# Kernel tuning notes

Measured on AMD Instinct MI355X. Metric: run time of the kernel, lower is better.

## Reference

```python
import jax, jax.numpy as jnp
import numpy as np

ANCHORS = np.array([[116., 90.], [156., 198.], [373., 326.],
                    [30., 61.], [62., 45.], [59., 119.],
                    [10., 13.], [16., 30.], [33., 23.]], dtype=np.float32)
IMG_WH = (416.0, 416.0)  # image_size[::-1]
IGNORE_THRESH = 0.5
MAX_BOXES = 64  # static upper bound on true boxes per image per layer


def bce_logits(t, x):
    # tf.nn.sigmoid_cross_entropy_with_logits(labels=t, logits=x)
    return jnp.maximum(x, 0.0) - x * t + jnp.log1p(jnp.exp(-jnp.abs(x)))


def box_iou(b1, b2):
    # b1: [B,H,W,3,4] xywh, b2: [B,M,4] xywh -> iou [B,H,W,3,M]
    b1 = b1[..., None, :]
    b2 = b2[:, None, None, None, :, :]
    b1_min = b1[..., :2] - b1[..., 2:4] * 0.5
    b1_max = b1[..., :2] + b1[..., 2:4] * 0.5
    b2_min = b2[..., :2] - b2[..., 2:4] * 0.5
    b2_max = b2[..., :2] + b2[..., 2:4] * 0.5
    inter_wh = jnp.maximum(jnp.minimum(b1_max, b2_max) - jnp.maximum(b1_min, b2_min), 0.0)
    inter = inter_wh[..., 0] * inter_wh[..., 1]
    a1 = b1[..., 2] * b1[..., 3]
    a2 = b2[..., 2] * b2[..., 3]
    return inter / (a1 + a2 - inter)


def layer_loss(yt, pred, anchors):
    # yt: [B,H,W,3,5+C], pred: [B,H,W,3*(5+C)]
    B, H, W = yt.shape[:3]
    C = pred.shape[-1] // 3 - 5
    p = pred.reshape(B, H, W, 3, 5 + C)
    gy, gx = jnp.meshgrid(jnp.arange(H), jnp.arange(W), indexing='ij')
    grid = jnp.stack([gx, gy], -1).astype(pred.dtype)[:, :, None, :]  # [H,W,1,2]
    fwh = jnp.array([W, H], pred.dtype)
    anc = anchors.reshape(1, 1, 1, 3, 2)
    # pred_process (channel layout: 0=conf, 1:3=xy, 3:5=wh, 5:=class)
    xy = (jax.nn.sigmoid(p[..., 1:3]) + grid) / fwh
    wh = jnp.exp(p[..., 3:5]) * anc / fwh
    conf = jax.nn.sigmoid(p[..., 0:1])
    cls = jax.nn.sigmoid(p[..., 5:])
    pred_box = jnp.concatenate([xy, wh], -1)

    obj = yt[..., 0:1]
    true_cls = yt[..., 5:]
    true_xy = yt[..., 1:3] * fwh - grid
    true_wh = jnp.log(yt[..., 3:5] / anc * jnp.array(IMG_WH, yt.dtype))
    true_wh = jnp.where(obj > 0, true_wh, jnp.zeros_like(true_wh))
    scale = 2.0 - yt[..., 3:4] * yt[..., 4:5]

    # vectorized replacement for the per-image while_loop + boolean_mask:
    # gather the MAX_BOXES highest-objectness cells per image as candidate true boxes
    flat_obj = obj[..., 0].reshape(B, -1)
    flat_box = yt[..., 1:5].reshape(B, -1, 4)
    vals, idx = jax.lax.top_k(flat_obj, MAX_BOXES)
    tboxes = jnp.take_along_axis(flat_box, idx[..., None], axis=1)  # [B,M,4]
    iou = box_iou(pred_box, tboxes)                                 # [B,H,W,3,M]
    iou = jnp.where((vals > 0.5)[:, None, None, None, :], iou, -jnp.inf)
    best_iou = jnp.max(iou, axis=-1)  # -inf when no true boxes (matches tf reduce_max over empty)
    ignore = (best_iou < IGNORE_THRESH).astype(yt.dtype)[..., None]

    xy_l = obj * scale * bce_logits(true_xy, xy)
    wh_l = obj * scale * 0.5 * jnp.square(true_wh - wh)
    conf_l = obj * bce_logits(obj, conf) + (1.0 - obj) * bce_logits(obj, conf) * ignore
    cls_l = obj * bce_logits(true_cls, cls)
    red = lambda t: jnp.sum(t, axis=(1, 2, 3, 4))
    return red(xy_l) + red(wh_l) + red(conf_l) + red(cls_l)


def yolo_loss(y_true, p0, p1, p2):
    B, _, A, D = y_true.shape
    yts = [y_true[:, 0:169].reshape(B, 13, 13, A, D),
           y_true[:, 169:845].reshape(B, 26, 26, A, D),
           y_true[:, 845:3549].reshape(B, 52, 52, A, D)]
    anc = jnp.asarray(ANCHORS)
    total = jnp.zeros((B,), y_true.dtype)
    for i, pred in enumerate([p0, p1, p2]):
        total = total + layer_loss(yts[i], pred, anc[3 * i:3 * i + 3])
    return total


def setup_inputs() -> dict:
    key = jax.random.key(0)
    B, N, C = 32, 3549, 80
    k1, k2, k3, k4, k5, k6, k7 = jax.random.split(key, 7)
    obj = (jax.random.uniform(k1, (B, N, 3, 1)) < 0.002).astype(jnp.float32)
    xy = jax.random.uniform(k2, (B, N, 3, 2), minval=0.05, maxval=0.95)
    wh = jax.random.uniform(k3, (B, N, 3, 2), minval=0.05, maxval=0.4)
    cls = (jax.random.uniform(k4, (B, N, 3, C)) < (1.0 / C)).astype(jnp.float32)
    y_true = jnp.concatenate([obj, xy, wh, cls], axis=-1)
    pred_13 = 0.5 * jax.random.normal(k5, (B, 13, 13, 255), dtype=jnp.float32)
    pred_26 = 0.5 * jax.random.normal(k6, (B, 26, 26, 255), dtype=jnp.float32)
    pred_52 = 0.5 * jax.random.normal(k7, (B, 52, 52, 255), dtype=jnp.float32)
    return {"y_true": y_true, "pred_13": pred_13, "pred_26": pred_26, "pred_52": pred_52}


def reference(y_true, pred_13, pred_26, pred_52):
    return yolo_loss(y_true, pred_13, pred_26, pred_52)
```

## Files before the change

### kernel.cpp

```cpp
#include <hip/hip_runtime.h>

#define NPAIR 96
#define MAXB 64
#define CAP 256

__constant__ float c_anc[9][2] = {
    {116.f, 90.f}, {156.f, 198.f}, {373.f, 326.f},
    { 30.f, 61.f}, { 62.f, 45.f}, { 59.f, 119.f},
    { 10.f, 13.f}, { 16.f, 30.f}, { 33.f, 23.f}};

typedef float floatx4 __attribute__((ext_vector_type(4), aligned(4)));

__device__ __forceinline__ float sigm(float x) { return 1.f / (1.f + expf(-x)); }

__device__ __forceinline__ float bce_f(float t, float x) {
    return fmaxf(x, 0.f) - x * t + logf(1.f + expf(-fabsf(x)));
}

__device__ __forceinline__ void map_block(int j, int& l, int& blk, int& S) {
    if (j < 2)       { l = 0; blk = j;      S = 13; }
    else if (j < 10) { l = 1; blk = j - 2;  S = 26; }
    else             { l = 2; blk = j - 10; S = 52; }
}

template <int ITERS>
__device__ __forceinline__ void scan_obj(const float* __restrict__ ybase,
                                         int nCells, int tid,
                                         unsigned long long* swords) {
    float ov[ITERS];
#pragma unroll
    for (int k = 0; k < ITERS; ++k) {
        int c = tid + (k << 8);
        ov[k] = (c < nCells) ? ybase[(long long)c * 85] : 0.f;
    }
    int lane = tid & 63, wv = tid >> 6;
#pragma unroll
    for (int k = 0; k < ITERS; ++k) {
        unsigned long long m = __ballot(ov[k] > 0.5f);
        if (lane == 0) swords[k * 4 + wv] = m;
    }
}

__global__ __launch_bounds__(256) void prep_k(
    const float* __restrict__ yt,
    const float* __restrict__ p13, const float* __restrict__ p26,
    const float* __restrict__ p52,
    float4* __restrict__ oboxes, int* __restrict__ counts,
    unsigned long long* __restrict__ bmp_all,
    float* __restrict__ posloss, float* __restrict__ out)
{
    int pair = blockIdx.x;
    int tid = threadIdx.x;
    int b = pair / 3;
    int l = pair - b * 3;
    int S      = (l == 0) ? 13  : (l == 1) ? 26  : 52;
    int n0     = (l == 0) ? 0   : (l == 1) ? 169 : 845;
    int nwords = (l == 0) ? 8   : (l == 1) ? 32  : 128;
    int nCells = S * S * 3;
    float Sf = (float)S;
    const float* ybase = yt + (long long)(b * 3549 + n0) * 255;
    const float* pred  = (l == 0) ? p13 : (l == 1) ? p26 : p52;
    const float* pbase = pred + (long long)b * S * S * 255;

    if (pair == 0 && tid < 32) out[tid] = 0.f;

    __shared__ unsigned long long swords[128];
    __shared__ int sidx[CAP];
    __shared__ int sbase[2];
    __shared__ int stot_s;
    __shared__ float pls[4];

    if (l == 0)      scan_obj<2 >(ybase, nCells, tid, swords);
    else if (l == 1) scan_obj<8 >(ybase, nCells, tid, swords);
    else             scan_obj<32>(ybase, nCells, tid, swords);
    __syncthreads();

    int lane = tid & 63, wv = tid >> 6;
    unsigned long long w = 0ULL;
    int pc = 0;
    if (tid < 128) {
        w = (tid < nwords) ? swords[tid] : 0ULL;
        pc = __popcll(w);
    }
    int x = pc;
#pragma unroll
    for (int d = 1; d < 64; d <<= 1) {
        int y = __shfl_up(x, d, 64);
        if (lane >= d) x += y;
    }
    if (tid < 128 && lane == 63) sbase[wv] = x;
    if (tid < nwords) bmp_all[(long long)pair * 128 + tid] = w;
    __syncthreads();
    if (tid == 0) stot_s = sbase[0] + sbase[1];
    if (tid < 128) {
        int base = x - pc + (wv ? sbase[0] : 0);
        unsigned long long ww = w;
        while (ww) {
            int bit = __ffsll((long long)ww) - 1;
            if (base < CAP) sidx[base] = tid * 64 + bit;
            ++base;
            ww &= ww - 1;
        }
    }
    __syncthreads();

    int stot = stot_s;
    int TC = stot < CAP ? stot : CAP;
    int MB = TC < MAXB ? TC : MAXB;
    if (tid == 0) counts[pair] = MB;
    if (tid < MB) {
        int idx = sidx[tid];
        const float* yc = ybase + (long long)idx * 85;
        oboxes[pair * MAXB + tid] = make_float4(yc[1], yc[2], yc[3], yc[4]);
    }

    float wsum = 0.f;
    for (int i = wv; i < TC; i += 4) {
        int idx = sidx[i];
        const float* yc = ybase + (long long)idx * 85;
        const float* pc_ = pbase + (long long)idx * 85;
        float part = bce_f(yc[5 + lane], sigm(pc_[5 + lane]));
        if (lane < 16)
            part += bce_f(yc[69 + lane], sigm(pc_[69 + lane]));
        if (lane == 0) {
            int p_ = idx / 3, a = idx - p_ * 3;
            int gh = p_ / S, gw = p_ - gh * S;
            float aw = c_anc[l * 3 + a][0], ah = c_anc[l * 3 + a][1];
            float v0 = pc_[0], v1 = pc_[1], v2 = pc_[2], v3 = pc_[3], v4 = pc_[4];
            float t1 = yc[1], t2 = yc[2], t3 = yc[3], t4 = yc[4];
            part += bce_f(1.f, sigm(v0));
            float sc = 2.f - t3 * t4;
            float px = (sigm(v1) + (float)gw) / Sf;
            float py = (sigm(v2) + (float)gh) / Sf;
            part += sc * (bce_f(t1 * Sf - (float)gw, px) +
                          bce_f(t2 * Sf - (float)gh, py));
            float pw = expf(v3) * aw / Sf, ph = expf(v4) * ah / Sf;
            float twx = logf(t3 / aw * 416.f), twy = logf(t4 / ah * 416.f);
            part += sc * 0.5f * ((twx - pw) * (twx - pw) + (twy - ph) * (twy - ph));
        }
#pragma unroll
        for (int off = 32; off > 0; off >>= 1)
            part += __shfl_down(part, off, 64);
        if (lane == 0) wsum += part;
    }
    if (lane == 0) pls[wv] = wsum;
    __syncthreads();
    if (tid == 0) posloss[pair] = pls[0] + pls[1] + pls[2] + pls[3];
}

__global__ __launch_bounds__(256) void neg_k(
    const float* __restrict__ p13, const float* __restrict__ p26,
    const float* __restrict__ p52,
    const float4* __restrict__ oboxes, const int* __restrict__ counts,
    const unsigned long long* __restrict__ bmp_all,
    const float* __restrict__ posloss, float* __restrict__ out)
{
    int bid = blockIdx.x;
    int tid = threadIdx.x;
    int b = bid / 42;
    int j = bid - b * 42;
    int l, blk, S;
    map_block(j, l, blk, S);
    int nCells = S * S * 3;
    int pair = b * 3 + l;
    float Sf = (float)S;
    const float* pred  = (l == 0) ? p13 : (l == 1) ? p26 : p52;
    const float* pbase = pred + (long long)b * S * S * 255;

    __shared__ float sxmin[MAXB], sxmax[MAXB], symin[MAXB], symax[MAXB], sba[MAXB];
    int count = counts[pair];
    if (tid < count) {
        float4 g = oboxes[pair * MAXB + tid];
        sxmin[tid] = g.x - g.z * 0.5f;
        sxmax[tid] = g.x + g.z * 0.5f;
        symin[tid] = g.y - g.w * 0.5f;
        symax[tid] = g.y + g.w * 0.5f;
        sba[tid]   = g.z * g.w;
    }
    __syncthreads();

    float loss = 0.f;
    int c = blk * 256 + tid;
    if (c < nCells) {
        unsigned long long word = bmp_all[(long long)pair * 128 + (c >> 6)];
        if (!((word >> (c & 63)) & 1ULL)) {
            const float* pc = pbase + (long long)c * 85;
            floatx4 v03 = *(const floatx4*)pc;
            float v0 = v03.x;
            if (count == 0) {
                loss = bce_f(0.f, sigm(v0));
            } else {
                float v4 = pc[4];
                int p_ = c / 3, a = c - p_ * 3;
                int gh = p_ / S, gw = p_ - gh * S;
                float aw = c_anc[l * 3 + a][0], ah = c_anc[l * 3 + a][1];
                float px = (sigm(v03.y) + (float)gw) / Sf;
                float py = (sigm(v03.z) + (float)gh) / Sf;
                float pw = expf(v03.w) * aw / Sf, ph = expf(v4) * ah / Sf;
                float pxmin = px - pw * 0.5f, pxmax = px + pw * 0.5f;
                float pymin = py - ph * 0.5f, pymax = py + ph * 0.5f;
                float parea = pw * ph;
                bool hit = false;
#pragma unroll 4
                for (int i = 0; i < count; ++i) {
                    float iw = fminf(pxmax, sxmax[i]) - fmaxf(pxmin, sxmin[i]);
                    float ih = fminf(pymax, symax[i]) - fmaxf(pymin, symin[i]);
                    float inter = fmaxf(iw, 0.f) * fmaxf(ih, 0.f);
                    hit = hit || (3.f * inter >= parea + sba[i]);
                }
                if (!hit) loss = bce_f(0.f, sigm(v0));
            }
        }
    }
    if (tid == 0 && blk == 0) loss += posloss[pair];

#pragma unroll
    for (int off = 32; off > 0; off >>= 1)
        loss += __shfl_down(loss, off, 64);
    __shared__ float wsum[4];
    if ((tid & 63) == 0) wsum[tid >> 6] = loss;
    __syncthreads();
    if (tid == 0)
        atomicAdd(out + b, wsum[0] + wsum[1] + wsum[2] + wsum[3]);
}

extern "C" void kernel_launch(void* const* d_in, const int* in_sizes, int n_in,
                              void* d_out, int out_size, void* d_ws, size_t ws_size,
                              hipStream_t stream) {
    (void)in_sizes; (void)n_in; (void)out_size; (void)ws_size;
    const float* yt  = (const float*)d_in[0];
    const float* p13 = (const float*)d_in[1];
    const float* p26 = (const float*)d_in[2];
    const float* p52 = (const float*)d_in[3];
    float* out = (float*)d_out;

    unsigned long long* bmp = (unsigned long long*)d_ws;
    float4* oboxes = (float4*)((char*)d_ws + NPAIR * 128 * 8);
    int* counts    = (int*)((char*)d_ws + NPAIR * 128 * 8 + NPAIR * MAXB * 16);
    float* posloss = (float*)((char*)d_ws + NPAIR * 128 * 8 + NPAIR * MAXB * 16
                              + NPAIR * sizeof(int));

    prep_k<<<NPAIR, 256, 0, stream>>>(yt, p13, p26, p52, oboxes, counts, bmp,
                                      posloss, out);
    neg_k<<<32 * 42, 256, 0, stream>>>(p13, p26, p52, oboxes, counts, bmp,
                                       posloss, out);
}
```

Baseline: 259.8 us.

## Fuse prep and negative-loss kernels, recomputing objectness scan per block

Merges the two-kernel pipeline into one kernel launched over 1344 blocks. Each block redoes the per-(image, layer) objectness scan and box gather in shared memory instead of reading them from a workspace written by a 96-block prep kernel. The positive-cell loss is computed only by block 0 of each pair. This removes the serial, low-occupancy prep stage and the workspace round trip, but repeats the strided y_true scan in every block of a layer (up to 32 blocks for the 52x52 layer). It also switches to fast __expf, __logf and rcp intrinsics and adds a tiny init kernel to zero the output.

```diff
diff --git a/kernel.cpp b/kernel.cpp
--- a/kernel.cpp
+++ b/kernel.cpp
@@ -1,6 +1,5 @@
 #include <hip/hip_runtime.h>
 
-#define NPAIR 96
 #define MAXB 64
 #define CAP 256
 
@@ -11,89 +10,88 @@
 
 typedef float floatx4 __attribute__((ext_vector_type(4), aligned(4)));
 
-__device__ __forceinline__ float sigm(float x) { return 1.f / (1.f + expf(-x)); }
-
+__device__ __forceinline__ float sigm(float x) {
+    return __builtin_amdgcn_rcpf(1.f + __expf(-x));
+}
 __device__ __forceinline__ float bce_f(float t, float x) {
-    return fmaxf(x, 0.f) - x * t + logf(1.f + expf(-fabsf(x)));
+    return fmaxf(x, 0.f) - x * t + __logf(1.f + __expf(-fabsf(x)));
 }
 
-__device__ __forceinline__ void map_block(int j, int& l, int& blk, int& S) {
-    if (j < 2)       { l = 0; blk = j;      S = 13; }
-    else if (j < 10) { l = 1; blk = j - 2;  S = 26; }
-    else             { l = 2; blk = j - 10; S = 52; }
+__device__ __forceinline__ void map_block(int j, int& l, int& blk, int& S,
+                                          int& n0, int& nwords) {
+    if (j < 2)       { l = 0; blk = j;      S = 13; n0 = 0;   nwords = 8;   }
+    else if (j < 10) { l = 1; blk = j - 2;  S = 26; n0 = 169; nwords = 32;  }
+    else             { l = 2; blk = j - 10; S = 52; n0 = 845; nwords = 128; }
 }
 
 template <int ITERS>
 __device__ __forceinline__ void scan_obj(const float* __restrict__ ybase,
-                                         int nCells, int tid,
+                                         int nCells, int lane, int wv,
                                          unsigned long long* swords) {
     float ov[ITERS];
 #pragma unroll
     for (int k = 0; k < ITERS; ++k) {
-        int c = tid + (k << 8);
+        int c = (((k << 2) + wv) << 6) + lane;
         ov[k] = (c < nCells) ? ybase[(long long)c * 85] : 0.f;
     }
-    int lane = tid & 63, wv = tid >> 6;
 #pragma unroll
     for (int k = 0; k < ITERS; ++k) {
         unsigned long long m = __ballot(ov[k] > 0.5f);
-        if (lane == 0) swords[k * 4 + wv] = m;
+        if (lane == 0) swords[(k << 2) + wv] = m;
     }
 }
 
-__global__ __launch_bounds__(256) void prep_k(
+__global__ void init_k(float* __restrict__ out) { out[threadIdx.x] = 0.f; }
+
+__global__ __launch_bounds__(256) void loss_k(
     const float* __restrict__ yt,
     const float* __restrict__ p13, const float* __restrict__ p26,
-    const float* __restrict__ p52,
-    float4* __restrict__ oboxes, int* __restrict__ counts,
-    unsigned long long* __restrict__ bmp_all,
-    float* __restrict__ posloss, float* __restrict__ out)
+    const float* __restrict__ p52, float* __restrict__ out)
 {
-    int pair = blockIdx.x;
-    int tid = threadIdx.x;
-    int b = pair / 3;
-    int l = pair - b * 3;
-    int S      = (l == 0) ? 13  : (l == 1) ? 26  : 52;
-    int n0     = (l == 0) ? 0   : (l == 1) ? 169 : 845;
-    int nwords = (l == 0) ? 8   : (l == 1) ? 32  : 128;
+    int bid = blockIdx.x, tid = threadIdx.x;
+    int b = bid / 42, j = bid - b * 42;
+    int l, blk, S, n0, nwords;
+    map_block(j, l, blk, S, n0, nwords);
     int nCells = S * S * 3;
     float Sf = (float)S;
+    float invS = __builtin_amdgcn_rcpf(Sf);
     const float* ybase = yt + (long long)(b * 3549 + n0) * 255;
     const float* pred  = (l == 0) ? p13 : (l == 1) ? p26 : p52;
     const float* pbase = pred + (long long)b * S * S * 255;
+    int lane = tid & 63, wv = tid >> 6;
 
-    if (pair == 0 && tid < 32) out[tid] = 0.f;
+    int c = blk * 256 + tid;
+    bool act = c < nCells;
+    int cc = act ? c : 0;
+    const float* pcp = pbase + (long long)cc * 85;
+    floatx4 v03 = *(const floatx4*)pcp;
+    float v4 = pcp[4];
 
     __shared__ unsigned long long swords[128];
     __shared__ int sidx[CAP];
-    __shared__ int sbase[2];
+    __shared__ int sbase2[2];
     __shared__ int stot_s;
-    __shared__ float pls[4];
+    __shared__ float sxmin[MAXB], sxmax[MAXB], symin[MAXB], symax[MAXB], sba[MAXB];
 
-    if (l == 0)      scan_obj<2 >(ybase, nCells, tid, swords);
-    else if (l == 1) scan_obj<8 >(ybase, nCells, tid, swords);
-    else             scan_obj<32>(ybase, nCells, tid, swords);
+    if (l == 0)      scan_obj<2 >(ybase, nCells, lane, wv, swords);
+    else if (l == 1) scan_obj<8 >(ybase, nCells, lane, wv, swords);
+    else             scan_obj<32>(ybase, nCells, lane, wv, swords);
     __syncthreads();
 
-    int lane = tid & 63, wv = tid >> 6;
     unsigned long long w = 0ULL;
     int pc = 0;
-    if (tid < 128) {
-        w = (tid < nwords) ? swords[tid] : 0ULL;
-        pc = __popcll(w);
-    }
+    if (tid < 128) { w = (tid < nwords) ? swords[tid] : 0ULL; pc = __popcll(w); }
     int x = pc;
 #pragma unroll
     for (int d = 1; d < 64; d <<= 1) {
         int y = __shfl_up(x, d, 64);
         if (lane >= d) x += y;
     }
-    if (tid < 128 && lane == 63) sbase[wv] = x;
-    if (tid < nwords) bmp_all[(long long)pair * 128 + tid] = w;
+    if (tid < 128 && lane == 63) sbase2[wv] = x;
     __syncthreads();
-    if (tid == 0) stot_s = sbase[0] + sbase[1];
+    if (tid == 0) stot_s = sbase2[0] + sbase2[1];
     if (tid < 128) {
-        int base = x - pc + (wv ? sbase[0] : 0);
+        int base = x - pc + (wv ? sbase2[0] : 0);
         unsigned long long ww = w;
         while (ww) {
             int bit = __ffsll((long long)ww) - 1;
@@ -107,141 +105,95 @@
     int stot = stot_s;
     int TC = stot < CAP ? stot : CAP;
     int MB = TC < MAXB ? TC : MAXB;
-    if (tid == 0) counts[pair] = MB;
     if (tid < MB) {
         int idx = sidx[tid];
+        if (idx >= nCells) idx = nCells - 1;
         const float* yc = ybase + (long long)idx * 85;
-        oboxes[pair * MAXB + tid] = make_float4(yc[1], yc[2], yc[3], yc[4]);
-    }
-
-    float wsum = 0.f;
-    for (int i = wv; i < TC; i += 4) {
-        int idx = sidx[i];
-        const float* yc = ybase + (long long)idx * 85;
-        const float* pc_ = pbase + (long long)idx * 85;
-        float part = bce_f(yc[5 + lane], sigm(pc_[5 + lane]));
-        if (lane < 16)
-            part += bce_f(yc[69 + lane], sigm(pc_[69 + lane]));
-        if (lane == 0) {
-            int p_ = idx / 3, a = idx - p_ * 3;
-            int gh = p_ / S, gw = p_ - gh * S;
-            float aw = c_anc[l * 3 + a][0], ah = c_anc[l * 3 + a][1];
-            float v0 = pc_[0], v1 = pc_[1], v2 = pc_[2], v3 = pc_[3], v4 = pc_[4];
-            float t1 = yc[1], t2 = yc[2], t3 = yc[3], t4 = yc[4];
-            part += bce_f(1.f, sigm(v0));
-            float sc = 2.f - t3 * t4;
-            float px = (sigm(v1) + (float)gw) / Sf;
-            float py = (sigm(v2) + (float)gh) / Sf;
-            part += sc * (bce_f(t1 * Sf - (float)gw, px) +
-                          bce_f(t2 * Sf - (float)gh, py));
-            float pw = expf(v3) * aw / Sf, ph = expf(v4) * ah / Sf;
-            float twx = logf(t3 / aw * 416.f), twy = logf(t4 / ah * 416.f);
-            part += sc * 0.5f * ((twx - pw) * (twx - pw) + (twy - ph) * (twy - ph));
-        }
-#pragma unroll
-        for (int off = 32; off > 0; off >>= 1)
-            part += __shfl_down(part, off, 64);
-        if (lane == 0) wsum += part;
-    }
-    if (lane == 0) pls[wv] = wsum;
-    __syncthreads();
-    if (tid == 0) posloss[pair] = pls[0] + pls[1] + pls[2] + pls[3];
-}
-
-__global__ __launch_bounds__(256) void neg_k(
-    const float* __restrict__ p13, const float* __restrict__ p26,
-    const float* __restrict__ p52,
-    const float4* __restrict__ oboxes, const int* __restrict__ counts,
-    const unsigned long long* __restrict__ bmp_all,
-    const float* __restrict__ posloss, float* __restrict__ out)
-{
-    int bid = blockIdx.x;
-    int tid = threadIdx.x;
-    int b = bid / 42;
-    int j = bid - b * 42;
-    int l, blk, S;
-    map_block(j, l, blk, S);
-    int nCells = S * S * 3;
-    int pair = b * 3 + l;
-    float Sf = (float)S;
-    const float* pred  = (l == 0) ? p13 : (l == 1) ? p26 : p52;
-    const float* pbase = pred + (long long)b * S * S * 255;
-
-    __shared__ float sxmin[MAXB], sxmax[MAXB], symin[MAXB], symax[MAXB], sba[MAXB];
-    int count = counts[pair];
-    if (tid < count) {
-        float4 g = oboxes[pair * MAXB + tid];
-        sxmin[tid] = g.x - g.z * 0.5f;
-        sxmax[tid] = g.x + g.z * 0.5f;
-        symin[tid] = g.y - g.w * 0.5f;
-        symax[tid] = g.y + g.w * 0.5f;
-        sba[tid]   = g.z * g.w;
+        float gx = yc[1], gy = yc[2], gww = yc[3], ghh = yc[4];
+        sxmin[tid] = gx - gww * 0.5f; sxmax[tid] = gx + gww * 0.5f;
+        symin[tid] = gy - ghh * 0.5f; symax[tid] = gy + ghh * 0.5f;
+        sba[tid]   = gww * ghh;
     }
     __syncthreads();
 
-    float loss = 0.f;
-    int c = blk * 256 + tid;
-    if (c < nCells) {
-        unsigned long long word = bmp_all[(long long)pair * 128 + (c >> 6)];
-        if (!((word >> (c & 63)) & 1ULL)) {
-            const float* pc = pbase + (long long)c * 85;
-            floatx4 v03 = *(const floatx4*)pc;
-            float v0 = v03.x;
-            if (count == 0) {
-                loss = bce_f(0.f, sigm(v0));
-            } else {
-                float v4 = pc[4];
-                int p_ = c / 3, a = c - p_ * 3;
-                int gh = p_ / S, gw = p_ - gh * S;
-                float aw = c_anc[l * 3 + a][0], ah = c_anc[l * 3 + a][1];
-                float px = (sigm(v03.y) + (float)gw) / Sf;
-                float py = (sigm(v03.z) + (float)gh) / Sf;
-                float pw = expf(v03.w) * aw / Sf, ph = expf(v4) * ah / Sf;
-                float pxmin = px - pw * 0.5f, pxmax = px + pw * 0.5f;
-                float pymin = py - ph * 0.5f, pymax = py + ph * 0.5f;
-                float parea = pw * ph;
-                bool hit = false;
-#pragma unroll 4
-                for (int i = 0; i < count; ++i) {
-                    float iw = fminf(pxmax, sxmax[i]) - fmaxf(pxmin, sxmin[i]);
-                    float ih = fminf(pymax, symax[i]) - fmaxf(pymin, symin[i]);
-                    float inter = fmaxf(iw, 0.f) * fmaxf(ih, 0.f);
-                    hit = hit || (3.f * inter >= parea + sba[i]);
-                }
-                if (!hit) loss = bce_f(0.f, sigm(v0));
+    int p_ = cc / 3, a = cc - p_ * 3;
+    int gh = p_ / S, gw = p_ - gh * S;
+    float aw = c_anc[l * 3 + a][0], ah = c_anc[l * 3 + a][1];
+    float px = (sigm(v03.y) + (float)gw) * invS;
+    float py = (sigm(v03.z) + (float)gh) * invS;
+    float pw = __expf(v03.w) * aw * invS, ph = __expf(v4) * ah * invS;
+    float pxmin = px - pw * 0.5f, pxmax = px + pw * 0.5f;
+    float pymin = py - ph * 0.5f, pymax = py + ph * 0.5f;
+    float parea = pw * ph;
+    bool hit = false;
+    for (int i = 0; i < MB; ++i) {
+        float iw = fminf(pxmax, sxmax[i]) - fmaxf(pxmin, sxmin[i]);
+        float ih = fminf(pymax, symax[i]) - fmaxf(pymin, symin[i]);
+        float inter = fmaxf(iw, 0.f) * fmaxf(ih, 0.f);
+        hit = hit || (3.f * inter >= parea + sba[i]);
+    }
+    bool posbit = (swords[cc >> 6] >> (cc & 63)) & 1ULL;
+    float conf = sigm(v03.x);
+    float bval = fmaxf(conf, 0.f) + __logf(1.f + __expf(-fabsf(conf)));
+    float loss = (act && !posbit && !hit) ? bval : 0.f;
+
+    if (blk == 0) {
+        float wsum = 0.f;
+        for (int i = wv; i < TC; i += 4) {
+            int idx = sidx[i];
+            if (idx >= nCells) idx = nCells - 1;
+            const float* yc = ybase + (long long)idx * 85;
+            const float* pp = pbase + (long long)idx * 85;
+            float part = bce_f(yc[5 + lane], sigm(pp[5 + lane]));
+            if (lane < 16)
+                part += bce_f(yc[69 + lane], sigm(pp[69 + lane]));
+            if (lane == 0) {
+                int q = idx / 3, aa = idx - q * 3;
+                int qh = q / S, qw = q - qh * S;
+                float aw2 = c_anc[l * 3 + aa][0], ah2 = c_anc[l * 3 + aa][1];
+                float t1 = yc[1], t2 = yc[2], t3 = yc[3], t4 = yc[4];
+                float u0 = pp[0], u1 = pp[1], u2 = pp[2], u3 = pp[3], u4 = pp[4];
+                part += bce_f(1.f, sigm(u0));
+                float sc = 2.f - t3 * t4;
+                float qx = (sigm(u1) + (float)qw) * invS;
+                float qy = (sigm(u2) + (float)qh) * invS;
+                part += sc * (bce_f(t1 * Sf - (float)qw, qx) +
+                              bce_f(t2 * Sf - (float)qh, qy));
+                float qpw = __expf(u3) * aw2 * invS;
+                float qph = __expf(u4) * ah2 * invS;
+                float twx = __logf(t3 / aw2 * 416.f);
+                float twy = __logf(t4 / ah2 * 416.f);
+                part += sc * 0.5f *
+                        ((twx - qpw) * (twx - qpw) + (twy - qph) * (twy - qph));
             }
+#pragma unroll
+            for (int off = 32; off > 0; off >>= 1)
+                part += __shfl_down(part, off, 64);
+            if (lane == 0) wsum += part;
         }
+        if (lane == 0) loss += wsum;
     }
-    if (tid == 0 && blk == 0) loss += posloss[pair];
 
 #pragma unroll
     for (int off = 32; off > 0; off >>= 1)
         loss += __shfl_down(loss, off, 64);
-    __shared__ float wsum[4];
-    if ((tid & 63) == 0) wsum[tid >> 6] = loss;
+    __shared__ float wred[4];
+    if (lane == 0) wred[wv] = loss;
     __syncthreads();
     if (tid == 0)
-        atomicAdd(out + b, wsum[0] + wsum[1] + wsum[2] + wsum[3]);
+        atomicAdd(out + b, wred[0] + wred[1] + wred[2] + wred[3]);
 }
 
 extern "C" void kernel_launch(void* const* d_in, const int* in_sizes, int n_in,
                               void* d_out, int out_size, void* d_ws, size_t ws_size,
                               hipStream_t stream) {
-    (void)in_sizes; (void)n_in; (void)out_size; (void)ws_size;
+    (void)in_sizes; (void)n_in; (void)out_size; (void)d_ws; (void)ws_size;
     const float* yt  = (const float*)d_in[0];
     const float* p13 = (const float*)d_in[1];
     const float* p26 = (const float*)d_in[2];
     const float* p52 = (const float*)d_in[3];
     float* out = (float*)d_out;
 
-    unsigned long long* bmp = (unsigned long long*)d_ws;
-    float4* oboxes = (float4*)((char*)d_ws + NPAIR * 128 * 8);
-    int* counts    = (int*)((char*)d_ws + NPAIR * 128 * 8 + NPAIR * MAXB * 16);
-    float* posloss = (float*)((char*)d_ws + NPAIR * 128 * 8 + NPAIR * MAXB * 16
-                              + NPAIR * sizeof(int));
-
-    prep_k<<<NPAIR, 256, 0, stream>>>(yt, p13, p26, p52, oboxes, counts, bmp,
-                                      posloss, out);
-    neg_k<<<32 * 42, 256, 0, stream>>>(p13, p26, p52, oboxes, counts, bmp,
-                                       posloss, out);
+    init_k<<<1, 32, 0, stream>>>(out);
+    loss_k<<<32 * 42, 256, 0, stream>>>(yt, p13, p26, p52, out);
 }
```

Result: slower. 265.2 us (+2.1%).
